# Kernel tuning notes

Measured on AMD Instinct MI355X. Metric: run time of the kernel, lower is better.

The kernel has to match this reference:

```python
import jax, jax.numpy as jnp
import numpy as np

EPS = 1e-08
TOP_K_PERCENT = 0.3


def _stft_mag(x, n_fft, hop):
    # torch.stft defaults: center=True (reflect pad n_fft//2), window=None (rect), onesided
    pad = n_fft // 2
    xp = jnp.pad(x, ((0, 0), (pad, pad)), mode='reflect')
    n_frames = 1 + (xp.shape[-1] - n_fft) // hop
    idx = jnp.arange(n_frames)[:, None] * hop + jnp.arange(n_fft)[None, :]
    frames = xp[:, idx]                       # [B, T, n_fft]
    spec = jnp.fft.rfft(frames, axis=-1)      # [B, T, F]
    mag = jnp.abs(spec).swapaxes(-1, -2)      # [B, F, T]
    return jnp.maximum(mag, EPS)


def _patchify(m, ps):
    # same patch partition as torch unfold/unfold/reshape (within-patch element
    # order differs but only per-patch means are consumed)
    B, F, T = m.shape
    pf = (-F) % ps
    pt = (-T) % ps
    mp = jnp.pad(m, ((0, 0), (0, pf), (0, pt)))
    nF, nT = (F + pf) // ps, (T + pt) // ps
    return mp.reshape(B, nF, ps, nT, ps).transpose(0, 1, 3, 2, 4).reshape(B, nF * nT, ps * ps)


def setup_inputs() -> dict:
    key = jax.random.key(0)
    ks, kt, kg = jax.random.split(key, 3)
    B, L = 16, 262144
    return {
        'student_waveform': jax.random.normal(ks, (B, L), dtype=jnp.float32),
        'teacher_waveform': jax.random.normal(kt, (B, L), dtype=jnp.float32),
        'target_waveform': jax.random.normal(kg, (B, L), dtype=jnp.float32),
        'n_fft': 1024,
        'hop_length': 256,
        'patch_size': 16,
    }


def reference(student_waveform, teacher_waveform, target_waveform, n_fft, hop_length, patch_size):
    s_mag = _stft_mag(student_waveform, n_fft, hop_length)
    t_mag = _stft_mag(teacher_waveform, n_fft, hop_length)
    g_mag = _stft_mag(target_waveform, n_fft, hop_length)

    s_p = _patchify(s_mag, patch_size)   # [B, P, ps*ps]
    t_p = _patchify(t_mag, patch_size)
    g_p = _patchify(g_mag, patch_size)

    err_s = jnp.mean(jnp.abs(s_p - g_p), axis=-1)   # [B, P]
    err_t = jnp.mean(jnp.abs(t_p - g_p), axis=-1)
    kgs = err_s - err_t
    patch_loss = jnp.mean((s_p - t_p) ** 2, axis=-1)

    B, P = patch_loss.shape
    k = max(1, int(P * TOP_K_PERCENT))
    _, idx = jax.lax.top_k(kgs, k)                   # [B, k]
    mask = jnp.zeros_like(kgs).at[jnp.arange(B)[:, None], idx].set(1.0)
    selected = jnp.sum(patch_loss * mask, axis=1)
    count = jnp.maximum(jnp.sum(mask, axis=1), 1.0)
    loss = jnp.mean(selected / count)

    sel_ratio = jnp.mean(mask)
    kgs_mean = jnp.mean(kgs)
    kgs_pos_ratio = jnp.mean((kgs > 0).astype(jnp.float32))
    return loss, sel_ratio, kgs_mean, kgs_pos_ratio
```

## Files before the change

### kernel.cpp

```cpp
#include <hip/hip_runtime.h>
#include <hip/hip_bf16.h>
#include <math.h>

#define BATCH 16
#define LEN   262144
#define NFFT  1024
#define HOP   256
#define PADW  512
#define NFREQ 513
#define NFRM  1025
#define PS    16
#define NPT   65
#define NPATCH 2145
#define TOPK  643
#define EPSV  1e-8f

#define SW(i) ((i) ^ (((i) >> 4) & 15))

__global__ __launch_bounds__(256) void stft_mag_kernel(
    const float* __restrict__ s_in,
    const float* __restrict__ t_in,
    const float* __restrict__ g_in,
    float* __restrict__ mag)
{
    __shared__ float2 xs[1024];
    __shared__ float2 tw[768];

    const int tid = threadIdx.x;
    const int p   = blockIdx.x;
    const int b   = blockIdx.y;
    const int w   = blockIdx.z;

    const float* src = (w == 0) ? s_in : (w == 1) ? t_in : g_in;
    src += (size_t)b * LEN;

    {
        float sv, cv;
        sincosf(-6.283185307179586476925f * (float)tid * (1.0f / 1024.0f), &sv, &cv);
        tw[SW(tid)]       = make_float2(cv, sv);
        tw[SW(tid + 256)] = make_float2(sv, -cv);
        tw[SW(tid + 512)] = make_float2(-cv, -sv);
    }

    const bool hasB  = (2 * p + 1) < NFRM;
    const int startA = 2 * p * HOP - PADW;

    #pragma unroll
    for (int m = 0; m < 4; ++m) {
        const int i = tid + 256 * m;
        int ga = startA + i;
        ga = (ga < 0) ? -ga : ga;
        ga = (ga >= LEN) ? (2 * LEN - 2 - ga) : ga;
        float re = src[ga];
        float im = 0.0f;
        if (hasB) {
            int gb = startA + HOP + i;
            gb = (gb < 0) ? -gb : gb;
            gb = (gb >= LEN) ? (2 * LEN - 2 - gb) : gb;
            im = src[gb];
        }
        xs[SW(i)] = make_float2(re, im);
    }
    __syncthreads();

    #pragma unroll
    for (int s = 0; s < 5; ++s) {
        const int lenlog = 10 - 2 * s;
        const int q      = 1 << (lenlog - 2);
        const int pos    = tid & (q - 1);
        const int blk    = tid >> (lenlog - 2);
        const int i0     = (blk << lenlog) + pos;

        float2 a  = xs[SW(i0)];
        float2 bb = xs[SW(i0 + q)];
        float2 c  = xs[SW(i0 + 2 * q)];
        float2 d  = xs[SW(i0 + 3 * q)];

        const float t0x = a.x + c.x,  t0y = a.y + c.y;
        const float t1x = a.x - c.x,  t1y = a.y - c.y;
        const float t2x = bb.x + d.x, t2y = bb.y + d.y;
        const float t3x = bb.x - d.x, t3y = bb.y - d.y;

        const float y0x = t0x + t2x, y0y = t0y + t2y;
        const float y1x = t1x + t3y, y1y = t1y - t3x;
        const float y2x = t0x - t2x, y2y = t0y - t2y;
        const float y3x = t1x - t3y, y3y = t1y + t3x;

        const int e  = pos << (2 * s);
        const float2 w1 = tw[SW(e)];
        const float2 w2 = tw[SW(2 * e)];
        const float2 w3 = tw[SW(3 * e)];

        xs[SW(i0)]         = make_float2(y0x, y0y);
        xs[SW(i0 + q)]     = make_float2(y1x * w1.x - y1y * w1.y, y1x * w1.y + y1y * w1.x);
        xs[SW(i0 + 2 * q)] = make_float2(y2x * w2.x - y2y * w2.y, y2x * w2.y + y2y * w2.x);
        xs[SW(i0 + 3 * q)] = make_float2(y3x * w3.x - y3y * w3.y, y3x * w3.y + y3y * w3.x);
        __syncthreads();
    }

    float* outA = mag + (((size_t)w * BATCH + b) * NFRM + 2 * p) * NFREQ;
    for (int k = tid; k < NFREQ; k += 256) {
        const unsigned rk = __brev((unsigned)k) >> 22;
        const unsigned pk = ((rk & 0x155u) << 1) | ((rk & 0x2AAu) >> 1);
        const unsigned mI = (unsigned)(1024 - k) & 1023u;
        const unsigned rm = __brev(mI) >> 22;
        const unsigned pm = ((rm & 0x155u) << 1) | ((rm & 0x2AAu) >> 1);
        const float2 Zk = xs[SW(pk)];
        const float2 Zm = xs[SW(pm)];
        const float ar = Zk.x + Zm.x, ai = Zk.y - Zm.y;
        const float br = Zk.y + Zm.y, bi = Zk.x - Zm.x;
        outA[k] = fmaxf(0.5f * sqrtf(ar * ar + ai * ai), EPSV);
        if (hasB) outA[NFREQ + k] = fmaxf(0.5f * sqrtf(br * br + bi * bi), EPSV);
    }
}

__global__ __launch_bounds__(256) void patch_stats_kernel(
    const float* __restrict__ mag,
    float* __restrict__ kgs,
    float* __restrict__ pl)
{
    const int tid = threadIdx.x;
    const int p   = blockIdx.x;
    const int b   = blockIdx.y;
    const int fi  = p / NPT;
    const int ti  = p - fi * NPT;
    const int f   = fi * PS + (tid & 15);
    const int t   = ti * PS + (tid >> 4);

    float sv = 0.0f, tv = 0.0f, gv = 0.0f;
    if (f < NFREQ && t < NFRM) {
        const size_t WOFF = (size_t)BATCH * NFRM * NFREQ;
        const size_t base = ((size_t)b * NFRM + t) * NFREQ + f;
        sv = mag[base];
        tv = mag[base + WOFF];
        gv = mag[base + 2 * WOFF];
    }
    float as = fabsf(sv - gv);
    float at = fabsf(tv - gv);
    float sq = (sv - tv) * (sv - tv);

    #pragma unroll
    for (int off = 32; off > 0; off >>= 1) {
        as += __shfl_down(as, off);
        at += __shfl_down(at, off);
        sq += __shfl_down(sq, off);
    }
    __shared__ float red[3][4];
    if ((tid & 63) == 0) {
        const int wv = tid >> 6;
        red[0][wv] = as; red[1][wv] = at; red[2][wv] = sq;
    }
    __syncthreads();
    if (tid == 0) {
        float sas = red[0][0] + red[0][1] + red[0][2] + red[0][3];
        float sat = red[1][0] + red[1][1] + red[1][2] + red[1][3];
        float ssq = red[2][0] + red[2][1] + red[2][2] + red[2][3];
        kgs[b * NPATCH + p] = (sas - sat) * (1.0f / 256.0f);
        pl [b * NPATCH + p] = ssq * (1.0f / 256.0f);
    }
}

__global__ __launch_bounds__(256) void topk_kernel(
    const float* __restrict__ kgs,
    const float* __restrict__ pl,
    float* __restrict__ rowstats)
{
    __shared__ unsigned ukey[NPATCH];
    __shared__ unsigned hist[256];
    __shared__ int      tIdx[NPATCH];
    __shared__ int      tcnt;
    __shared__ unsigned selByte;
    __shared__ float    red[3][4];

    const int tid = threadIdx.x;
    const int b   = blockIdx.x;
    const float* row = kgs + b * NPATCH;
    const float* plrow = pl + b * NPATCH;

    float lsum = 0.0f, lpos = 0.0f;
    for (int i = tid; i < NPATCH; i += 256) {
        float v = row[i];
        lsum += v;
        lpos += (v > 0.0f) ? 1.0f : 0.0f;
        unsigned u = __float_as_uint(v);
        u = (u & 0x80000000u) ? ~u : (u | 0x80000000u);
        ukey[i] = u;
    }
    __syncthreads();

    unsigned prefix = 0;
    int rem = TOPK;
    #pragma unroll
    for (int pass = 0; pass < 4; ++pass) {
        const int shift = 24 - 8 * pass;
        const unsigned himask = (pass == 0) ? 0u : (0xFFFFFFFFu << (shift + 8));

        hist[tid] = 0;
        __syncthreads();
        for (int i = tid; i < NPATCH; i += 256) {
            unsigned u = ukey[i];
            if ((u & himask) == (prefix & himask))
                atomicAdd(&hist[(u >> shift) & 255u], 1u);
        }
        __syncthreads();
        for (int off = 1; off < 256; off <<= 1) {
            unsigned v = (tid + off < 256) ? hist[tid + off] : 0u;
            __syncthreads();
            hist[tid] += v;
            __syncthreads();
        }
        unsigned sb  = hist[tid];
        unsigned sb1 = (tid == 255) ? 0u : hist[tid + 1];
        if (sb >= (unsigned)rem && sb1 < (unsigned)rem) selByte = (unsigned)tid;
        __syncthreads();
        const unsigned B = selByte;
        rem -= (int)((B == 255u) ? 0u : hist[B + 1]);
        prefix |= (B << shift);
        __syncthreads();
    }

    const unsigned T = prefix;
    float ssum = 0.0f;
    if (tid == 0) tcnt = 0;
    __syncthreads();
    for (int i = tid; i < NPATCH; i += 256) {
        unsigned u = ukey[i];
        if (u > T) {
            ssum += plrow[i];
        } else if (u == T) {
            int j = atomicAdd(&tcnt, 1);
            tIdx[j] = i;
        }
    }
    __syncthreads();
    const int m = tcnt;
    if (m == rem) {
        for (int j = tid; j < m; j += 256) ssum += plrow[tIdx[j]];
    } else {
        for (int j = tid; j < m; j += 256) {
            const int i = tIdx[j];
            int rank = 0;
            for (int q = 0; q < m; ++q) rank += (tIdx[q] < i) ? 1 : 0;
            if (rank < rem) ssum += plrow[i];
        }
    }

    #pragma unroll
    for (int off = 32; off > 0; off >>= 1) {
        ssum += __shfl_down(ssum, off);
        lsum += __shfl_down(lsum, off);
        lpos += __shfl_down(lpos, off);
    }
    if ((tid & 63) == 0) {
        const int wv = tid >> 6;
        red[0][wv] = ssum; red[1][wv] = lsum; red[2][wv] = lpos;
    }
    __syncthreads();
    if (tid == 0) {
        rowstats[b * 3 + 0] = red[0][0] + red[0][1] + red[0][2] + red[0][3];
        rowstats[b * 3 + 1] = red[1][0] + red[1][1] + red[1][2] + red[1][3];
        rowstats[b * 3 + 2] = red[2][0] + red[2][1] + red[2][2] + red[2][3];
    }
}

__global__ __launch_bounds__(64) void final_kernel(
    const float* __restrict__ rowstats,
    float* __restrict__ out)
{
    const int tid = threadIdx.x;
    float loss = 0.0f, ks = 0.0f, pc = 0.0f;
    if (tid < BATCH) {
        loss = rowstats[tid * 3 + 0] * (1.0f / (float)TOPK);
        ks   = rowstats[tid * 3 + 1];
        pc   = rowstats[tid * 3 + 2];
    }
    #pragma unroll
    for (int off = 32; off > 0; off >>= 1) {
        loss += __shfl_down(loss, off);
        ks   += __shfl_down(ks, off);
        pc   += __shfl_down(pc, off);
    }
    if (tid == 0) {
        out[0] = loss * (1.0f / (float)BATCH);
        out[1] = (float)TOPK / (float)NPATCH;
        out[2] = ks * (1.0f / ((float)BATCH * (float)NPATCH));
        out[3] = pc * (1.0f / ((float)BATCH * (float)NPATCH));
    }
}

extern "C" void kernel_launch(void* const* d_in, const int* in_sizes, int n_in,
                              void* d_out, int out_size, void* d_ws, size_t ws_size,
                              hipStream_t stream)
{
    const float* s_in = (const float*)d_in[0];
    const float* t_in = (const float*)d_in[1];
    const float* g_in = (const float*)d_in[2];
    float* out = (float*)d_out;

    const size_t magElems = (size_t)3 * BATCH * NFRM * NFREQ;
    float* mag = (float*)d_ws;
    float* kgs = mag + magElems;
    float* pl  = kgs + (size_t)BATCH * NPATCH;
    float* rowstats = pl + (size_t)BATCH * NPATCH;

    dim3 g1(513, BATCH, 3);
    stft_mag_kernel<<<g1, 256, 0, stream>>>(s_in, t_in, g_in, mag);

    dim3 g2(NPATCH, BATCH, 1);
    patch_stats_kernel<<<g2, 256, 0, stream>>>(mag, kgs, pl);

    topk_kernel<<<BATCH, 256, 0, stream>>>(kgs, pl, rowstats);

    final_kernel<<<1, 64, 0, stream>>>(rowstats, out);
}
```

Before: 212.8 us.

## Fuse STFT magnitude and patch statistics into one kernel, dropping spectrogram buffer

Each block now processes one 16-frame time column of patches for one batch row. It computes the STFT magnitudes for all three signals in shared memory and accumulates per-patch error sums directly, so the full magnitude spectrogram is no longer written to and reread from global memory. Twiddles w2/w3 are derived from w1 arithmetically, and the top-k radix scan uses wavefront shuffles with pl cached in LDS. The trade-off is far fewer blocks, each running 24 sequential FFTs, which lowers parallelism and latency hiding.

```diff
diff --git a/kernel.cpp b/kernel.cpp
--- a/kernel.cpp
+++ b/kernel.cpp
@@ -4,65 +4,38 @@
 
 #define BATCH 16
 #define LEN   262144
-#define NFFT  1024
 #define HOP   256
 #define PADW  512
 #define NFREQ 513
 #define NFRM  1025
-#define PS    16
 #define NPT   65
+#define NPF   33
 #define NPATCH 2145
 #define TOPK  643
 #define EPSV  1e-8f
 
 #define SW(i) ((i) ^ (((i) >> 4) & 15))
 
-__global__ __launch_bounds__(256) void stft_mag_kernel(
-    const float* __restrict__ s_in,
-    const float* __restrict__ t_in,
-    const float* __restrict__ g_in,
-    float* __restrict__ mag)
-{
-    __shared__ float2 xs[1024];
-    __shared__ float2 tw[768];
-
-    const int tid = threadIdx.x;
-    const int p   = blockIdx.x;
-    const int b   = blockIdx.y;
-    const int w   = blockIdx.z;
-
-    const float* src = (w == 0) ? s_in : (w == 1) ? t_in : g_in;
-    src += (size_t)b * LEN;
-
-    {
-        float sv, cv;
-        sincosf(-6.283185307179586476925f * (float)tid * (1.0f / 1024.0f), &sv, &cv);
-        tw[SW(tid)]       = make_float2(cv, sv);
-        tw[SW(tid + 256)] = make_float2(sv, -cv);
-        tw[SW(tid + 512)] = make_float2(-cv, -sv);
-    }
-
-    const bool hasB  = (2 * p + 1) < NFRM;
-    const int startA = 2 * p * HOP - PADW;
-
+__device__ __forceinline__ int reflect_idx(int g) {
+    g = (g < 0) ? -g : g;
+    g = (g >= LEN) ? (2 * LEN - 2 - g) : g;
+    return g;
+}
+
+__device__ __forceinline__ void load_pack(float2* xs,
+    const float* __restrict__ re_src, const float* __restrict__ im_src,
+    int startRe, int startIm, int tid)
+{
     #pragma unroll
     for (int m = 0; m < 4; ++m) {
         const int i = tid + 256 * m;
-        int ga = startA + i;
-        ga = (ga < 0) ? -ga : ga;
-        ga = (ga >= LEN) ? (2 * LEN - 2 - ga) : ga;
-        float re = src[ga];
-        float im = 0.0f;
-        if (hasB) {
-            int gb = startA + HOP + i;
-            gb = (gb < 0) ? -gb : gb;
-            gb = (gb >= LEN) ? (2 * LEN - 2 - gb) : gb;
-            im = src[gb];
-        }
-        xs[SW(i)] = make_float2(re, im);
-    }
-    __syncthreads();
-
+        xs[SW(i)] = make_float2(re_src[reflect_idx(startRe + i)],
+                                im_src[reflect_idx(startIm + i)]);
+    }
+    __syncthreads();
+}
+
+__device__ __forceinline__ void fft1024(float2* xs, const float2* tw, int tid) {
     #pragma unroll
     for (int s = 0; s < 5; ++s) {
         const int lenlog = 10 - 2 * s;
@@ -86,10 +59,10 @@
         const float y2x = t0x - t2x, y2y = t0y - t2y;
         const float y3x = t1x - t3y, y3y = t1y + t3x;
 
-        const int e  = pos << (2 * s);
+        const int e = pos << (2 * s);
         const float2 w1 = tw[SW(e)];
-        const float2 w2 = tw[SW(2 * e)];
-        const float2 w3 = tw[SW(3 * e)];
+        const float2 w2 = make_float2(w1.x * w1.x - w1.y * w1.y, 2.0f * w1.x * w1.y);
+        const float2 w3 = make_float2(w2.x * w1.x - w2.y * w1.y, w2.x * w1.y + w2.y * w1.x);
 
         xs[SW(i0)]         = make_float2(y0x, y0y);
         xs[SW(i0 + q)]     = make_float2(y1x * w1.x - y1y * w1.y, y1x * w1.y + y1y * w1.x);
@@ -97,8 +70,11 @@
         xs[SW(i0 + 3 * q)] = make_float2(y3x * w3.x - y3y * w3.y, y3x * w3.y + y3y * w3.x);
         __syncthreads();
     }
-
-    float* outA = mag + (((size_t)w * BATCH + b) * NFRM + 2 * p) * NFREQ;
+}
+
+__device__ __forceinline__ void unpack_mags(const float2* xs,
+    float* __restrict__ magA, float* __restrict__ magB, int tid)
+{
     for (int k = tid; k < NFREQ; k += 256) {
         const unsigned rk = __brev((unsigned)k) >> 22;
         const unsigned pk = ((rk & 0x155u) << 1) | ((rk & 0x2AAu) >> 1);
@@ -109,54 +85,88 @@
         const float2 Zm = xs[SW(pm)];
         const float ar = Zk.x + Zm.x, ai = Zk.y - Zm.y;
         const float br = Zk.y + Zm.y, bi = Zk.x - Zm.x;
-        outA[k] = fmaxf(0.5f * sqrtf(ar * ar + ai * ai), EPSV);
-        if (hasB) outA[NFREQ + k] = fmaxf(0.5f * sqrtf(br * br + bi * bi), EPSV);
-    }
-}
-
-__global__ __launch_bounds__(256) void patch_stats_kernel(
-    const float* __restrict__ mag,
-    float* __restrict__ kgs,
-    float* __restrict__ pl)
-{
+        magA[k] = fmaxf(0.5f * sqrtf(ar * ar + ai * ai), EPSV);
+        magB[k] = fmaxf(0.5f * sqrtf(br * br + bi * bi), EPSV);
+    }
+    __syncthreads();
+}
+
+__global__ __launch_bounds__(256) void stft_patch_kernel(
+    const float* __restrict__ s_in, const float* __restrict__ t_in,
+    const float* __restrict__ g_in,
+    float* __restrict__ kgs, float* __restrict__ pl)
+{
+    __shared__ float2 xs[1024];
+    __shared__ float2 tw[256];
+    __shared__ float magS[2][516];
+    __shared__ float magT[2][516];
+    __shared__ float magG[2][516];
+    __shared__ float accAS[NPF], accAT[NPF], accSQ[NPF];
+
     const int tid = threadIdx.x;
-    const int p   = blockIdx.x;
+    const int ti  = blockIdx.x;
     const int b   = blockIdx.y;
-    const int fi  = p / NPT;
-    const int ti  = p - fi * NPT;
-    const int f   = fi * PS + (tid & 15);
-    const int t   = ti * PS + (tid >> 4);
-
-    float sv = 0.0f, tv = 0.0f, gv = 0.0f;
-    if (f < NFREQ && t < NFRM) {
-        const size_t WOFF = (size_t)BATCH * NFRM * NFREQ;
-        const size_t base = ((size_t)b * NFRM + t) * NFREQ + f;
-        sv = mag[base];
-        tv = mag[base + WOFF];
-        gv = mag[base + 2 * WOFF];
-    }
-    float as = fabsf(sv - gv);
-    float at = fabsf(tv - gv);
-    float sq = (sv - tv) * (sv - tv);
-
-    #pragma unroll
-    for (int off = 32; off > 0; off >>= 1) {
-        as += __shfl_down(as, off);
-        at += __shfl_down(at, off);
-        sq += __shfl_down(sq, off);
-    }
-    __shared__ float red[3][4];
-    if ((tid & 63) == 0) {
-        const int wv = tid >> 6;
-        red[0][wv] = as; red[1][wv] = at; red[2][wv] = sq;
-    }
-    __syncthreads();
-    if (tid == 0) {
-        float sas = red[0][0] + red[0][1] + red[0][2] + red[0][3];
-        float sat = red[1][0] + red[1][1] + red[1][2] + red[1][3];
-        float ssq = red[2][0] + red[2][1] + red[2][2] + red[2][3];
-        kgs[b * NPATCH + p] = (sas - sat) * (1.0f / 256.0f);
-        pl [b * NPATCH + p] = ssq * (1.0f / 256.0f);
+
+    const float* sp = s_in + (size_t)b * LEN;
+    const float* tp = t_in + (size_t)b * LEN;
+    const float* gp = g_in + (size_t)b * LEN;
+
+    {
+        float sv, cv;
+        sincosf(-6.283185307179586476925f * (float)tid * (1.0f / 1024.0f), &sv, &cv);
+        tw[SW(tid)] = make_float2(cv, sv);
+    }
+    if (tid < NPF) { accAS[tid] = 0.0f; accAT[tid] = 0.0f; accSQ[tid] = 0.0f; }
+    __syncthreads();
+
+    for (int u = 0; u < 8; ++u) {
+        const int tA = ti * 16 + 2 * u;
+        if (tA >= NFRM) break;
+        const int startA = tA * HOP - PADW;
+        const int startB = startA + HOP;
+
+        load_pack(xs, sp, tp, startA, startA, tid);
+        fft1024(xs, tw, tid);
+        unpack_mags(xs, magS[0], magT[0], tid);
+
+        load_pack(xs, sp, tp, startB, startB, tid);
+        fft1024(xs, tw, tid);
+        unpack_mags(xs, magS[1], magT[1], tid);
+
+        load_pack(xs, gp, gp, startA, startB, tid);
+        fft1024(xs, tw, tid);
+        unpack_mags(xs, magG[0], magG[1], tid);
+
+        #pragma unroll
+        for (int par = 0; par < 2; ++par) {
+            if (tA + par >= NFRM) break;
+            #pragma unroll
+            for (int it = 0; it < 3; ++it) {
+                const int f = tid + 256 * it;
+                float sm = 0.0f, tm = 0.0f, gm = 0.0f;
+                if (f < NFREQ) { sm = magS[par][f]; tm = magT[par][f]; gm = magG[par][f]; }
+                float as = fabsf(sm - gm);
+                float at = fabsf(tm - gm);
+                float sq = (sm - tm) * (sm - tm);
+                #pragma unroll
+                for (int off = 8; off >= 1; off >>= 1) {
+                    as += __shfl_down(as, off);
+                    at += __shfl_down(at, off);
+                    sq += __shfl_down(sq, off);
+                }
+                if ((tid & 15) == 0 && f < NFREQ) {
+                    const int g16 = f >> 4;
+                    accAS[g16] += as; accAT[g16] += at; accSQ[g16] += sq;
+                }
+            }
+        }
+    }
+    __syncthreads();
+
+    if (tid < NPF) {
+        const int p = tid * NPT + ti;
+        kgs[b * NPATCH + p] = (accAS[tid] - accAT[tid]) * (1.0f / 256.0f);
+        pl [b * NPATCH + p] = accSQ[tid] * (1.0f / 256.0f);
     }
 }
 
@@ -166,26 +176,29 @@
     float* __restrict__ rowstats)
 {
     __shared__ unsigned ukey[NPATCH];
+    __shared__ float    plv[NPATCH];
     __shared__ unsigned hist[256];
+    __shared__ unsigned wtot[4];
     __shared__ int      tIdx[NPATCH];
     __shared__ int      tcnt;
-    __shared__ unsigned selByte;
+    __shared__ unsigned selB, selHi;
     __shared__ float    red[3][4];
 
     const int tid = threadIdx.x;
     const int b   = blockIdx.x;
-    const float* row = kgs + b * NPATCH;
-    const float* plrow = pl + b * NPATCH;
+    const float* row   = kgs + b * NPATCH;
+    const float* plrow = pl  + b * NPATCH;
 
     float lsum = 0.0f, lpos = 0.0f;
     for (int i = tid; i < NPATCH; i += 256) {
         float v = row[i];
         lsum += v;
         lpos += (v > 0.0f) ? 1.0f : 0.0f;
+        plv[i] = plrow[i];
         unsigned u = __float_as_uint(v);
-        u = (u & 0x80000000u) ? ~u : (u | 0x80000000u);
-        ukey[i] = u;
-    }
+        ukey[i] = (u & 0x80000000u) ? ~u : (u | 0x80000000u);
+    }
+    if (tid == 0) tcnt = 0;
     __syncthreads();
 
     unsigned prefix = 0;
@@ -203,30 +216,35 @@
                 atomicAdd(&hist[(u >> shift) & 255u], 1u);
         }
         __syncthreads();
-        for (int off = 1; off < 256; off <<= 1) {
-            unsigned v = (tid + off < 256) ? hist[tid + off] : 0u;
-            __syncthreads();
-            hist[tid] += v;
-            __syncthreads();
-        }
-        unsigned sb  = hist[tid];
-        unsigned sb1 = (tid == 255) ? 0u : hist[tid + 1];
-        if (sb >= (unsigned)rem && sb1 < (unsigned)rem) selByte = (unsigned)tid;
-        __syncthreads();
-        const unsigned B = selByte;
-        rem -= (int)((B == 255u) ? 0u : hist[B + 1]);
-        prefix |= (B << shift);
+
+        const unsigned h = hist[tid];
+        unsigned v = h;
+        const int lane = tid & 63;
+        const int w    = tid >> 6;
+        #pragma unroll
+        for (int off = 1; off < 64; off <<= 1) {
+            unsigned tval = __shfl_down(v, off);
+            if (lane + off < 64) v += tval;
+        }
+        if (lane == 0) wtot[w] = v;
+        __syncthreads();
+        unsigned addv = 0;
+        for (int w2 = w + 1; w2 < 4; ++w2) addv += wtot[w2];
+        v += addv;
+        const unsigned hi = v - h;
+        if (v >= (unsigned)rem && hi < (unsigned)rem) { selB = (unsigned)tid; selHi = hi; }
+        __syncthreads();
+        prefix |= (selB << shift);
+        rem -= (int)selHi;
         __syncthreads();
     }
 
     const unsigned T = prefix;
     float ssum = 0.0f;
-    if (tid == 0) tcnt = 0;
-    __syncthreads();
     for (int i = tid; i < NPATCH; i += 256) {
         unsigned u = ukey[i];
         if (u > T) {
-            ssum += plrow[i];
+            ssum += plv[i];
         } else if (u == T) {
             int j = atomicAdd(&tcnt, 1);
             tIdx[j] = i;
@@ -235,13 +253,13 @@
     __syncthreads();
     const int m = tcnt;
     if (m == rem) {
-        for (int j = tid; j < m; j += 256) ssum += plrow[tIdx[j]];
+        for (int j = tid; j < m; j += 256) ssum += plv[tIdx[j]];
     } else {
         for (int j = tid; j < m; j += 256) {
             const int i = tIdx[j];
             int rank = 0;
             for (int q = 0; q < m; ++q) rank += (tIdx[q] < i) ? 1 : 0;
-            if (rank < rem) ssum += plrow[i];
+            if (rank < rem) ssum += plv[i];
         }
     }
 
@@ -297,17 +315,12 @@
     const float* g_in = (const float*)d_in[2];
     float* out = (float*)d_out;
 
-    const size_t magElems = (size_t)3 * BATCH * NFRM * NFREQ;
-    float* mag = (float*)d_ws;
-    float* kgs = mag + magElems;
+    float* kgs = (float*)d_ws;
     float* pl  = kgs + (size_t)BATCH * NPATCH;
     float* rowstats = pl + (size_t)BATCH * NPATCH;
 
-    dim3 g1(513, BATCH, 3);
-    stft_mag_kernel<<<g1, 256, 0, stream>>>(s_in, t_in, g_in, mag);
-
-    dim3 g2(NPATCH, BATCH, 1);
-    patch_stats_kernel<<<g2, 256, 0, stream>>>(mag, kgs, pl);
+    dim3 g1(NPT, BATCH);
+    stft_patch_kernel<<<g1, 256, 0, stream>>>(s_in, t_in, g_in, kgs, pl);
 
     topk_kernel<<<BATCH, 256, 0, stream>>>(kgs, pl, rowstats);
 
```

After: 227.5 us. 1.07x slower.
